# Kernel tuning notes

Measured on AMD Instinct MI355X. Metric: run time of the kernel, lower is better.

The kernel has to match this reference:

```python
import jax, jax.numpy as jnp
import numpy as np

B, N, C, H = 2, 2048, 1024, 16
HD = C // H
FF = 2 * C


def _layernorm(x, w, b, eps=1e-5):
    mu = jnp.mean(x, axis=-1, keepdims=True)
    var = jnp.var(x, axis=-1, keepdims=True)
    return (x - mu) * jax.lax.rsqrt(var + eps) * w + b


def setup_inputs() -> dict:
    key = jax.random.key(0)
    ks = jax.random.split(key, 16)
    std = 0.02
    d = {
        'q': jax.random.normal(ks[0], (B, N, C), jnp.float32),
        'k': jax.random.normal(ks[1], (B, N, C), jnp.float32),
        'v': jax.random.normal(ks[2], (B, N, C), jnp.float32),
        # attention projections (stored [in, out])
        'Wq': jax.random.normal(ks[3], (C, C), jnp.float32) * std,
        'bq': jnp.zeros((C,), jnp.float32),
        'Wk': jax.random.normal(ks[4], (C, C), jnp.float32) * std,
        'bk': jnp.zeros((C,), jnp.float32),
        'Wv': jax.random.normal(ks[5], (C, C), jnp.float32) * std,
        'bv': jnp.zeros((C,), jnp.float32),
        'Wo': jax.random.normal(ks[6], (C, C), jnp.float32) * std,
        'bo': jnp.zeros((C,), jnp.float32),
        # post-attention LayerNorm
        'ln_w': jnp.ones((C,), jnp.float32),
        'ln_b': jnp.zeros((C,), jnp.float32),
        # FFN
        'W1': jax.random.normal(ks[7], (C, FF), jnp.float32) * std,
        'b1': jnp.zeros((FF,), jnp.float32),
        'W2': jax.random.normal(ks[8], (FF, C), jnp.float32) * std,
        'b2': jnp.zeros((C,), jnp.float32),
    }
    return d


def reference(q, k, v, Wq, bq, Wk, bk, Wv, bv, Wo, bo, ln_w, ln_b, W1, b1, W2, b2):
    scale = HD ** -0.5
    # Note: the torch forward overwrites the normalized-input attention with
    # attention on raw q,k,v; only the second call affects the output.
    qh = (q @ Wq + bq).reshape(B, N, H, HD)  # [B,Nq,H,hd]
    kh = (k @ Wk + bk).reshape(B, N, H, HD)
    vh = (v @ Wv + bv).reshape(B, N, H, HD)
    attn = jnp.einsum('bqhd,bkhd->bhqk', qh, kh) * scale
    attn = jax.nn.softmax(attn, axis=-1)
    ctx = jnp.einsum('bhqk,bkhd->bqhd', attn, vh).reshape(B, N, C)
    x = ctx @ Wo + bo
    x = x + q  # residual (drop_path=0, dropout eval -> identity)
    h = _layernorm(x, ln_w, ln_b)
    y = jax.nn.gelu(h @ W1 + b1, approximate=False) @ W2 + b2
    return y + x
```

## Files before the change

kernel.cpp:

```cpp
#include <hip/hip_runtime.h>

constexpr int B_ = 2, N_ = 2048, C_ = 1024, H_ = 16, HD_ = 64, FF_ = 2048;

typedef __attribute__((ext_vector_type(8))) __bf16 bf16x8;
typedef __attribute__((ext_vector_type(4))) float f32x4;
typedef __attribute__((ext_vector_type(4))) short s16x4;

__device__ __forceinline__ unsigned short f2bf(float f) {
  union { float f; unsigned int u; } v; v.f = f;
  unsigned int r = v.u + 0x7fffu + ((v.u >> 16) & 1u);
  return (unsigned short)(r >> 16);
}

__device__ __forceinline__ void gload_lds16(const unsigned short* g, unsigned short* l) {
  __builtin_amdgcn_global_load_lds((const __attribute__((address_space(1))) void*)g,
                                   (__attribute__((address_space(3))) void*)l, 16, 0, 0);
}

__global__ __launch_bounds__(256)
void cast3_bf16(const float* __restrict__ q, const float* __restrict__ k,
                const float* __restrict__ v, unsigned short* __restrict__ qo,
                unsigned short* __restrict__ ko, unsigned short* __restrict__ vo, int n8) {
  int i = blockIdx.x * 256 + threadIdx.x;
  if (i >= n8) return;
  const float* in = blockIdx.z == 0 ? q : (blockIdx.z == 1 ? k : v);
  unsigned short* out = blockIdx.z == 0 ? qo : (blockIdx.z == 1 ? ko : vo);
  const float4 a = ((const float4*)in)[2 * i];
  const float4 b = ((const float4*)in)[2 * i + 1];
  uint4 o;
  o.x = (unsigned)f2bf(a.x) | ((unsigned)f2bf(a.y) << 16);
  o.y = (unsigned)f2bf(a.z) | ((unsigned)f2bf(a.w) << 16);
  o.z = (unsigned)f2bf(b.x) | ((unsigned)f2bf(b.y) << 16);
  o.w = (unsigned)f2bf(b.z) | ((unsigned)f2bf(b.w) << 16);
  ((uint4*)out)[i] = o;
}

__global__ __launch_bounds__(256)
void wt_cast(const float* __restrict__ W, unsigned short* __restrict__ Wt, int K, int N) {
  __shared__ unsigned short tile[32][33];
  const int tx = threadIdx.x, ty = threadIdx.y;
  const int n0 = blockIdx.x * 32, k0 = blockIdx.y * 32;
#pragma unroll
  for (int r = 0; r < 4; ++r)
    tile[ty + r * 8][tx] = f2bf(W[(size_t)(k0 + ty + r * 8) * N + n0 + tx]);
  __syncthreads();
#pragma unroll
  for (int r = 0; r < 4; ++r)
    Wt[(size_t)(n0 + ty + r * 8) * K + k0 + tx] = tile[tx][ty + r * 8];
}

__global__ __launch_bounds__(256)
void wt_cast4(const float* __restrict__ Wa, const float* __restrict__ Wb,
              const float* __restrict__ Wc, const float* __restrict__ Wd,
              unsigned short* __restrict__ Oa, unsigned short* __restrict__ Ob,
              unsigned short* __restrict__ Oc, unsigned short* __restrict__ Od) {
  __shared__ unsigned short tile[32][33];
  const int z = blockIdx.z;
  const float* W = z == 0 ? Wa : (z == 1 ? Wb : (z == 2 ? Wc : Wd));
  unsigned short* Wt = z == 0 ? Oa : (z == 1 ? Ob : (z == 2 ? Oc : Od));
  const int tx = threadIdx.x, ty = threadIdx.y;
  const int n0 = blockIdx.x * 32, k0 = blockIdx.y * 32;
#pragma unroll
  for (int r = 0; r < 4; ++r)
    tile[ty + r * 8][tx] = f2bf(W[(size_t)(k0 + ty + r * 8) * C_ + n0 + tx]);
  __syncthreads();
#pragma unroll
  for (int r = 0; r < 4; ++r)
    Wt[(size_t)(n0 + ty + r * 8) * C_ + k0 + tx] = tile[tx][ty + r * 8];
}

__global__ __launch_bounds__(256)
void vh_transpose(const unsigned short* __restrict__ Vh, unsigned short* __restrict__ VhT) {
  __shared__ unsigned short tile[32][33];
  const int tx = threadIdx.x, ty = threadIdx.y;
  const int bh = blockIdx.z, b = bh >> 4, h = bh & 15;
  const int n0 = blockIdx.x * 32, d0 = blockIdx.y * 32;
#pragma unroll
  for (int r = 0; r < 4; ++r) {
    int n = n0 + ty + r * 8;
    tile[ty + r * 8][tx] = Vh[((size_t)(b * N_ + n)) * C_ + h * HD_ + d0 + tx];
  }
  __syncthreads();
#pragma unroll
  for (int r = 0; r < 4; ++r) {
    int d = d0 + ty + r * 8;
    VhT[((size_t)(bh * HD_ + d)) * N_ + n0 + tx] = tile[tx][ty + r * 8];
  }
}

__global__ __launch_bounds__(256, 2)
void gemm_qkv(const unsigned short* __restrict__ A0, const unsigned short* __restrict__ A1,
              const unsigned short* __restrict__ A2, const unsigned short* __restrict__ B0,
              const unsigned short* __restrict__ B1, const unsigned short* __restrict__ B2,
              const float* __restrict__ c0, const float* __restrict__ c1v,
              const float* __restrict__ c2, unsigned short* __restrict__ O0,
              unsigned short* __restrict__ O1, unsigned short* __restrict__ O2) {
  const int z = blockIdx.z;
  const unsigned short* A = z == 0 ? A0 : (z == 1 ? A1 : A2);
  const unsigned short* Bt = z == 0 ? B0 : (z == 1 ? B1 : B2);
  const float* bias = z == 0 ? c0 : (z == 1 ? c1v : c2);
  unsigned short* outB = z == 0 ? O0 : (z == 1 ? O1 : O2);
  const int K = C_, Nn = C_;

  __shared__ unsigned short lA[128 * 64];
  __shared__ unsigned short lB[128 * 64];
  const int t = threadIdx.x;
  const int lane = t & 63;
  const int w = t >> 6;
  const int wm = w >> 1, wn = w & 1;
  const int l15 = lane & 15, g = lane >> 4;

  const unsigned short* Ab = A + (size_t)blockIdx.x * 128 * K;
  const unsigned short* Bb = Bt + (size_t)blockIdx.y * 128 * K;

  f32x4 acc[4][4] = {};

  for (int k0 = 0; k0 < K; k0 += 64) {
    __syncthreads();
#pragma unroll
    for (int i = 0; i < 4; ++i) {
      int id = i * 256 + t;
      gload_lds16(Ab + (size_t)(id >> 3) * K + k0 + (id & 7) * 8, &lA[id * 8]);
    }
#pragma unroll
    for (int i = 0; i < 4; ++i) {
      int id = i * 256 + t;
      gload_lds16(Bb + (size_t)(id >> 3) * K + k0 + (id & 7) * 8, &lB[id * 8]);
    }
    __syncthreads();
#pragma unroll
    for (int kk = 0; kk < 2; ++kk) {
      bf16x8 af[4], bfr[4];
#pragma unroll
      for (int mi = 0; mi < 4; ++mi)
        af[mi] = *(const bf16x8*)&lA[(wm * 64 + mi * 16 + l15) * 64 + kk * 32 + g * 8];
#pragma unroll
      for (int ni = 0; ni < 4; ++ni)
        bfr[ni] = *(const bf16x8*)&lB[(wn * 64 + ni * 16 + l15) * 64 + kk * 32 + g * 8];
#pragma unroll
      for (int mi = 0; mi < 4; ++mi)
#pragma unroll
        for (int ni = 0; ni < 4; ++ni)
          acc[mi][ni] = __builtin_amdgcn_mfma_f32_16x16x32_bf16(af[mi], bfr[ni], acc[mi][ni], 0, 0, 0);
    }
  }

#pragma unroll
  for (int mi = 0; mi < 4; ++mi)
#pragma unroll
    for (int ni = 0; ni < 4; ++ni) {
      const int col = blockIdx.y * 128 + wn * 64 + ni * 16 + l15;
      const float bcol = bias[col];
#pragma unroll
      for (int r = 0; r < 4; ++r) {
        const int row = blockIdx.x * 128 + wm * 64 + mi * 16 + g * 4 + r;
        outB[(size_t)row * Nn + col] = f2bf(acc[mi][ni][r] + bcol);
      }
    }
}

template <int EPI>
__global__ __launch_bounds__(256, 2)
void gemm_bt(const unsigned short* __restrict__ A, const unsigned short* __restrict__ Bt,
             const float* __restrict__ bias, const float* __restrict__ resid,
             float* __restrict__ outF, unsigned short* __restrict__ outB,
             int M, int N, int K) {
  __shared__ unsigned short lA[128 * 64];
  __shared__ unsigned short lB[128 * 64];
  const int t = threadIdx.x;
  const int lane = t & 63;
  const int w = t >> 6;
  const int wm = w >> 1, wn = w & 1;
  const int l15 = lane & 15, g = lane >> 4;

  const unsigned short* Ab = A + (size_t)blockIdx.x * 128 * K;
  const unsigned short* Bb = Bt + (size_t)blockIdx.y * 128 * K;

  f32x4 acc[4][4] = {};

  for (int k0 = 0; k0 < K; k0 += 64) {
    __syncthreads();
#pragma unroll
    for (int i = 0; i < 4; ++i) {
      int id = i * 256 + t;
      gload_lds16(Ab + (size_t)(id >> 3) * K + k0 + (id & 7) * 8, &lA[id * 8]);
    }
#pragma unroll
    for (int i = 0; i < 4; ++i) {
      int id = i * 256 + t;
      gload_lds16(Bb + (size_t)(id >> 3) * K + k0 + (id & 7) * 8, &lB[id * 8]);
    }
    __syncthreads();
#pragma unroll
    for (int kk = 0; kk < 2; ++kk) {
      bf16x8 af[4], bfr[4];
#pragma unroll
      for (int mi = 0; mi < 4; ++mi)
        af[mi] = *(const bf16x8*)&lA[(wm * 64 + mi * 16 + l15) * 64 + kk * 32 + g * 8];
#pragma unroll
      for (int ni = 0; ni < 4; ++ni)
        bfr[ni] = *(const bf16x8*)&lB[(wn * 64 + ni * 16 + l15) * 64 + kk * 32 + g * 8];
#pragma unroll
      for (int mi = 0; mi < 4; ++mi)
#pragma unroll
        for (int ni = 0; ni < 4; ++ni)
          acc[mi][ni] = __builtin_amdgcn_mfma_f32_16x16x32_bf16(af[mi], bfr[ni], acc[mi][ni], 0, 0, 0);
    }
  }

#pragma unroll
  for (int mi = 0; mi < 4; ++mi)
#pragma unroll
    for (int ni = 0; ni < 4; ++ni) {
      const int col = blockIdx.y * 128 + wn * 64 + ni * 16 + l15;
      const float bcol = bias[col];
#pragma unroll
      for (int r = 0; r < 4; ++r) {
        const int row = blockIdx.x * 128 + wm * 64 + mi * 16 + g * 4 + r;
        const size_t o = (size_t)row * N + col;
        float val = acc[mi][ni][r] + bcol;
        if (EPI == 0) {
          outB[o] = f2bf(val);
        } else if (EPI == 1) {
          outF[o] = val + resid[o];
        } else {
          float ge = 0.5f * val * (1.0f + erff(val * 0.70710678118654752f));
          outB[o] = f2bf(ge);
        }
      }
    }
}

__global__ __launch_bounds__(256, 2)
void gemm_n64(const unsigned short* __restrict__ A, const unsigned short* __restrict__ Bt,
              const float* __restrict__ bias, const float* __restrict__ resid,
              float* __restrict__ outF, int M, int N, int K) {
  __shared__ unsigned short lA[128 * 64];
  __shared__ unsigned short lB[64 * 64];
  const int t = threadIdx.x;
  const int lane = t & 63;
  const int w = t >> 6;
  const int wm = w >> 1, wn = w & 1;
  const int l15 = lane & 15, g = lane >> 4;

  const unsigned short* Ab = A + (size_t)blockIdx.x * 128 * K;
  const unsigned short* Bb = Bt + (size_t)blockIdx.y * 64 * K;

  f32x4 acc[4][2] = {};

  for (int k0 = 0; k0 < K; k0 += 64) {
    __syncthreads();
#pragma unroll
    for (int i = 0; i < 4; ++i) {
      int id = i * 256 + t;
      gload_lds16(Ab + (size_t)(id >> 3) * K + k0 + (id & 7) * 8, &lA[id * 8]);
    }
#pragma unroll
    for (int i = 0; i < 2; ++i) {
      int id = i * 256 + t;
      gload_lds16(Bb + (size_t)(id >> 3) * K + k0 + (id & 7) * 8, &lB[id * 8]);
    }
    __syncthreads();
#pragma unroll
    for (int kk = 0; kk < 2; ++kk) {
      bf16x8 af[4], bfr[2];
#pragma unroll
      for (int mi = 0; mi < 4; ++mi)
        af[mi] = *(const bf16x8*)&lA[(wm * 64 + mi * 16 + l15) * 64 + kk * 32 + g * 8];
#pragma unroll
      for (int ni = 0; ni < 2; ++ni)
        bfr[ni] = *(const bf16x8*)&lB[(wn * 32 + ni * 16 + l15) * 64 + kk * 32 + g * 8];
#pragma unroll
      for (int mi = 0; mi < 4; ++mi)
#pragma unroll
        for (int ni = 0; ni < 2; ++ni)
          acc[mi][ni] = __builtin_amdgcn_mfma_f32_16x16x32_bf16(af[mi], bfr[ni], acc[mi][ni], 0, 0, 0);
    }
  }

#pragma unroll
  for (int mi = 0; mi < 4; ++mi)
#pragma unroll
    for (int ni = 0; ni < 2; ++ni) {
      const int col = blockIdx.y * 64 + wn * 32 + ni * 16 + l15;
      const float bcol = bias[col];
#pragma unroll
      for (int r = 0; r < 4; ++r) {
        const int row = blockIdx.x * 128 + wm * 64 + mi * 16 + g * 4 + r;
        const size_t o = (size_t)row * N + col;
        outF[o] = acc[mi][ni][r] + bcol + resid[o];
      }
    }
}

__global__ __launch_bounds__(256, 2)
void attn_fwd(const unsigned short* __restrict__ Qh, const unsigned short* __restrict__ Kh,
              const unsigned short* __restrict__ VhT, unsigned short* __restrict__ ctx) {
  __shared__ unsigned short lK[2][64 * 64];
  __shared__ unsigned short lV[2][64 * 64];

  const int t = threadIdx.x, lane = t & 63, w = t >> 6;
  const int l15 = lane & 15, g = lane >> 4;
  const int bh = blockIdx.y, b = bh >> 4, h = bh & 15;
  const int qb0 = blockIdx.x * 128 + w * 32;

  const unsigned short* Qb = Qh + (size_t)b * N_ * C_ + h * HD_;
  const unsigned short* Kb = Kh + (size_t)b * N_ * C_ + h * HD_;
  const unsigned short* Vb = VhT + (size_t)bh * HD_ * N_;

  bf16x8 qf[2][2];
#pragma unroll
  for (int qi = 0; qi < 2; ++qi)
#pragma unroll
    for (int kk = 0; kk < 2; ++kk)
      qf[qi][kk] = *(const bf16x8*)(Qb + (size_t)(qb0 + qi * 16 + l15) * C_ + kk * 32 + g * 8);

  auto stageK = [&](int buf, int kb) {
#pragma unroll
    for (int i = 0; i < 2; ++i) {
      int o = (i * 256 + t) * 16;
      int r = o >> 7;
      int c = (o & 127) ^ ((r & 7) << 4);
      gload_lds16(Kb + (size_t)(kb + r) * C_ + (c >> 1), &lK[buf][o >> 1]);
    }
  };
  auto stageV = [&](int buf, int kb) {
#pragma unroll
    for (int i = 0; i < 2; ++i) {
      int o = (i * 256 + t) * 16;
      int r = o >> 7;
      int c = (o & 127) ^ ((r & 7) << 4);
      gload_lds16(Vb + (size_t)r * N_ + kb + (c >> 1), &lV[buf][o >> 1]);
    }
  };

  f32x4 od[4][2] = {};
  float mrun[2] = {-1e30f, -1e30f};
  float srun[2] = {0.f, 0.f};
  const float c1 = 0.18033688011112042f;
  const float DTHR = 8.0f / 0.18033688011112042f;

  stageK(0, 0);
  stageV(0, 0);
  __syncthreads();

  int cur = 0;
  for (int tile = 0; tile < N_ / 64; ++tile) {
    if (tile + 1 < N_ / 64) {
      stageK(cur ^ 1, (tile + 1) * 64);
      stageV(cur ^ 1, (tile + 1) * 64);
    }

    f32x4 st[4][2];
#pragma unroll
    for (int kf = 0; kf < 4; ++kf) {
      const int krow = kf * 16 + l15;
      const int sw = (krow & 7) << 4;
      const bf16x8 ka = *(const bf16x8*)&lK[cur][krow * 64 + ((( g * 16) ^ sw) >> 1)];
      const bf16x8 kc = *(const bf16x8*)&lK[cur][krow * 64 + (((64 + g * 16) ^ sw) >> 1)];
#pragma unroll
      for (int qi = 0; qi < 2; ++qi) {
        f32x4 z = {};
        z = __builtin_amdgcn_mfma_f32_16x16x32_bf16(ka, qf[qi][0], z, 0, 0, 0);
        z = __builtin_amdgcn_mfma_f32_16x16x32_bf16(kc, qf[qi][1], z, 0, 0, 0);
        st[kf][qi] = z;
      }
    }

    s16x4 pb[4][2];
#pragma unroll
    for (int qi = 0; qi < 2; ++qi) {
      float mx = st[0][qi][0];
#pragma unroll
      for (int r = 1; r < 4; ++r) mx = fmaxf(mx, st[0][qi][r]);
#pragma unroll
      for (int kf = 1; kf < 4; ++kf)
#pragma unroll
        for (int r = 0; r < 4; ++r) mx = fmaxf(mx, st[kf][qi][r]);
      mx = fmaxf(mx, __shfl_xor(mx, 16));
      mx = fmaxf(mx, __shfl_xor(mx, 32));
      if (__any(mx > mrun[qi] + DTHR)) {
        const float mn = fmaxf(mrun[qi], mx);
        const float sf = exp2f((mrun[qi] - mn) * c1);
        mrun[qi] = mn;
        srun[qi] *= sf;
#pragma unroll
        for (int di = 0; di < 4; ++di)
#pragma unroll
          for (int r = 0; r < 4; ++r) od[di][qi][r] *= sf;
      }
      const float mc = mrun[qi] * c1;
#pragma unroll
      for (int kf = 0; kf < 4; ++kf) {
        union { s16x4 v; __bf16 e[4]; } u;
#pragma unroll
        for (int r = 0; r < 4; ++r) {
          float pv = exp2f(st[kf][qi][r] * c1 - mc);
          srun[qi] += pv;
          u.e[r] = (__bf16)pv;
        }
        pb[kf][qi] = u.v;
      }
    }

#pragma unroll
    for (int di = 0; di < 4; ++di) {
      const int vrow = di * 16 + l15;
      const int sw = (vrow & 7) << 4;
#pragma unroll
      for (int kf = 0; kf < 4; ++kf) {
        const s16x4 vt = *(const s16x4*)&lV[cur][vrow * 64 + (((kf * 32 + g * 8) ^ sw) >> 1)];
#pragma unroll
        for (int qi = 0; qi < 2; ++qi)
          od[di][qi] = __builtin_amdgcn_mfma_f32_16x16x16bf16_1k(vt, pb[kf][qi], od[di][qi], 0, 0, 0);
      }
    }

    __syncthreads();
    cur ^= 1;
  }

#pragma unroll
  for (int qi = 0; qi < 2; ++qi) {
    float s = srun[qi];
    s += __shfl_xor(s, 16);
    s += __shfl_xor(s, 32);
    float rinv = 1.0f / s;
    const int q = qb0 + qi * 16 + l15;
#pragma unroll
    for (int di = 0; di < 4; ++di)
#pragma unroll
      for (int r = 0; r < 4; ++r) {
        int d = di * 16 + g * 4 + r;
        ctx[((size_t)(b * N_ + q)) * C_ + h * HD_ + d] = f2bf(od[di][qi][r] * rinv);
      }
  }
}

__global__ __launch_bounds__(256)
void ln_kernel(const float* __restrict__ x, const float* __restrict__ lw,
               const float* __restrict__ lb, unsigned short* __restrict__ h) {
  const int row = blockIdx.x;
  const int t = threadIdx.x;
  const float4 v = ((const float4*)(x + (size_t)row * C_))[t];
  float sum = v.x + v.y + v.z + v.w;
#pragma unroll
  for (int m = 1; m < 64; m <<= 1) sum += __shfl_xor(sum, m);
  __shared__ float red[8];
  if ((t & 63) == 0) red[t >> 6] = sum;
  __syncthreads();
  const float mu = (red[0] + red[1] + red[2] + red[3]) * (1.0f / C_);
  const float d0 = v.x - mu, d1 = v.y - mu, d2 = v.z - mu, d3 = v.w - mu;
  float sq = d0 * d0 + d1 * d1 + d2 * d2 + d3 * d3;
#pragma unroll
  for (int m = 1; m < 64; m <<= 1) sq += __shfl_xor(sq, m);
  if ((t & 63) == 0) red[4 + (t >> 6)] = sq;
  __syncthreads();
  const float var = (red[4] + red[5] + red[6] + red[7]) * (1.0f / C_);
  const float rstd = rsqrtf(var + 1e-5f);
  const float4 ww = ((const float4*)lw)[t];
  const float4 bb = ((const float4*)lb)[t];
  uint2 o;
  o.x = (unsigned)f2bf(d0 * rstd * ww.x + bb.x) | ((unsigned)f2bf(d1 * rstd * ww.y + bb.y) << 16);
  o.y = (unsigned)f2bf(d2 * rstd * ww.z + bb.z) | ((unsigned)f2bf(d3 * rstd * ww.w + bb.w) << 16);
  ((uint2*)(h + (size_t)row * C_))[t] = o;
}

extern "C" void kernel_launch(void* const* d_in, const int* in_sizes, int n_in,
                              void* d_out, int out_size, void* d_ws, size_t ws_size,
                              hipStream_t stream) {
  const float* q   = (const float*)d_in[0];
  const float* k   = (const float*)d_in[1];
  const float* v   = (const float*)d_in[2];
  const float* Wq  = (const float*)d_in[3];
  const float* bq  = (const float*)d_in[4];
  const float* Wk  = (const float*)d_in[5];
  const float* bk  = (const float*)d_in[6];
  const float* Wv  = (const float*)d_in[7];
  const float* bv  = (const float*)d_in[8];
  const float* Wo  = (const float*)d_in[9];
  const float* bo  = (const float*)d_in[10];
  const float* lnw = (const float*)d_in[11];
  const float* lnb = (const float*)d_in[12];
  const float* W1  = (const float*)d_in[13];
  const float* b1  = (const float*)d_in[14];
  const float* W2  = (const float*)d_in[15];
  const float* b2  = (const float*)d_in[16];
  float* out = (float*)d_out;

  char* ws = (char*)d_ws;
  const size_t MB = 1024 * 1024;
  if (ws_size < 120 * MB) return;
  unsigned short* qb   = (unsigned short*)(ws + 0 * MB);
  unsigned short* kb   = (unsigned short*)(ws + 8 * MB);
  unsigned short* vb   = (unsigned short*)(ws + 16 * MB);
  unsigned short* Wqt  = (unsigned short*)(ws + 24 * MB);
  unsigned short* Wkt  = (unsigned short*)(ws + 26 * MB);
  unsigned short* Wvt  = (unsigned short*)(ws + 28 * MB);
  unsigned short* Wot  = (unsigned short*)(ws + 30 * MB);
  unsigned short* W1t  = (unsigned short*)(ws + 32 * MB);
  unsigned short* W2t  = (unsigned short*)(ws + 36 * MB);
  unsigned short* Qh   = (unsigned short*)(ws + 40 * MB);
  unsigned short* Kh   = (unsigned short*)(ws + 48 * MB);
  unsigned short* Vh   = (unsigned short*)(ws + 56 * MB);
  unsigned short* VhT  = (unsigned short*)(ws + 64 * MB);
  unsigned short* ctx  = (unsigned short*)(ws + 72 * MB);
  float*          xf   = (float*)(ws + 80 * MB);
  unsigned short* hb   = (unsigned short*)(ws + 96 * MB);
  unsigned short* tbuf = (unsigned short*)(ws + 104 * MB);

  const int n8 = B_ * N_ * C_ / 8;
  cast3_bf16<<<dim3((n8 + 255) / 256, 1, 3), 256, 0, stream>>>(q, k, v, qb, kb, vb, n8);

  dim3 blk32(32, 8);
  wt_cast4<<<dim3(C_ / 32, C_ / 32, 4), blk32, 0, stream>>>(Wq, Wk, Wv, Wo, Wqt, Wkt, Wvt, Wot);
  wt_cast<<<dim3(FF_ / 32, C_ / 32), blk32, 0, stream>>>(W1, W1t, C_, FF_);
  wt_cast<<<dim3(C_ / 32, FF_ / 32), blk32, 0, stream>>>(W2, W2t, FF_, C_);

  gemm_qkv<<<dim3(B_ * N_ / 128, C_ / 128, 3), 256, 0, stream>>>(qb, kb, vb, Wqt, Wkt, Wvt,
                                                                 bq, bk, bv, Qh, Kh, Vh);

  vh_transpose<<<dim3(N_ / 32, HD_ / 32, B_ * H_), blk32, 0, stream>>>(Vh, VhT);
  attn_fwd<<<dim3(N_ / 128, B_ * H_), 256, 0, stream>>>(Qh, Kh, VhT, ctx);

  gemm_n64<<<dim3(B_ * N_ / 128, C_ / 64), 256, 0, stream>>>(ctx, Wot, bo, q, xf, B_ * N_, C_, C_);
  ln_kernel<<<dim3(B_ * N_), 256, 0, stream>>>(xf, lnw, lnb, hb);
  gemm_bt<2><<<dim3(B_ * N_ / 128, FF_ / 128), 256, 0, stream>>>(hb, W1t, b1, nullptr, nullptr, tbuf,
                                                                 B_ * N_, FF_, C_);
  gemm_n64<<<dim3(B_ * N_ / 128, C_ / 64), 256, 0, stream>>>(tbuf, W2t, b2, xf, out, B_ * N_, C_, FF_);
}
```

Measured before the change: 245.3 us.

## Double-buffer GEMM LDS tiles, add MFMA priority hints, enlarge attention blocks

All three GEMM kernels now use double-buffered LDS tiles, so the next K-slice is loaded while MFMAs run on the current one, with one barrier per iteration instead of two. s_setprio raises wave priority around the MFMA blocks in the GEMMs and in attention. The attention kernel moves to 512-thread blocks covering 256 queries, halving the K/V staging per thread and sharing each K/V tile across more waves. Its context output is written as packed 8-byte stores instead of scalar 2-byte stores. Doubling LDS per GEMM block (64KB for the 128x128 tiles) may reduce occupancy, and the larger attention blocks halve the grid size.

```diff
diff --git a/kernel.cpp b/kernel.cpp
--- a/kernel.cpp
+++ b/kernel.cpp
@@ -102,8 +102,8 @@
   unsigned short* outB = z == 0 ? O0 : (z == 1 ? O1 : O2);
   const int K = C_, Nn = C_;
 
-  __shared__ unsigned short lA[128 * 64];
-  __shared__ unsigned short lB[128 * 64];
+  __shared__ unsigned short lA[2][128 * 64];
+  __shared__ unsigned short lB[2][128 * 64];
   const int t = threadIdx.x;
   const int lane = t & 63;
   const int w = t >> 6;
@@ -113,36 +113,45 @@
   const unsigned short* Ab = A + (size_t)blockIdx.x * 128 * K;
   const unsigned short* Bb = Bt + (size_t)blockIdx.y * 128 * K;
 
-  f32x4 acc[4][4] = {};
-
-  for (int k0 = 0; k0 < K; k0 += 64) {
-    __syncthreads();
+  auto stage = [&](int buf, int k0) {
 #pragma unroll
     for (int i = 0; i < 4; ++i) {
       int id = i * 256 + t;
-      gload_lds16(Ab + (size_t)(id >> 3) * K + k0 + (id & 7) * 8, &lA[id * 8]);
+      gload_lds16(Ab + (size_t)(id >> 3) * K + k0 + (id & 7) * 8, &lA[buf][id * 8]);
     }
 #pragma unroll
     for (int i = 0; i < 4; ++i) {
       int id = i * 256 + t;
-      gload_lds16(Bb + (size_t)(id >> 3) * K + k0 + (id & 7) * 8, &lB[id * 8]);
-    }
-    __syncthreads();
+      gload_lds16(Bb + (size_t)(id >> 3) * K + k0 + (id & 7) * 8, &lB[buf][id * 8]);
+    }
+  };
+
+  f32x4 acc[4][4] = {};
+
+  stage(0, 0);
+  __syncthreads();
+  int cur = 0;
+  for (int k0 = 0; k0 < K; k0 += 64) {
+    if (k0 + 64 < K) stage(cur ^ 1, k0 + 64);
 #pragma unroll
     for (int kk = 0; kk < 2; ++kk) {
       bf16x8 af[4], bfr[4];
 #pragma unroll
       for (int mi = 0; mi < 4; ++mi)
-        af[mi] = *(const bf16x8*)&lA[(wm * 64 + mi * 16 + l15) * 64 + kk * 32 + g * 8];
+        af[mi] = *(const bf16x8*)&lA[cur][(wm * 64 + mi * 16 + l15) * 64 + kk * 32 + g * 8];
 #pragma unroll
       for (int ni = 0; ni < 4; ++ni)
-        bfr[ni] = *(const bf16x8*)&lB[(wn * 64 + ni * 16 + l15) * 64 + kk * 32 + g * 8];
+        bfr[ni] = *(const bf16x8*)&lB[cur][(wn * 64 + ni * 16 + l15) * 64 + kk * 32 + g * 8];
+      __builtin_amdgcn_s_setprio(1);
 #pragma unroll
       for (int mi = 0; mi < 4; ++mi)
 #pragma unroll
         for (int ni = 0; ni < 4; ++ni)
           acc[mi][ni] = __builtin_amdgcn_mfma_f32_16x16x32_bf16(af[mi], bfr[ni], acc[mi][ni], 0, 0, 0);
-    }
+      __builtin_amdgcn_s_setprio(0);
+    }
+    __syncthreads();
+    cur ^= 1;
   }
 
 #pragma unroll
@@ -165,8 +174,8 @@
              const float* __restrict__ bias, const float* __restrict__ resid,
              float* __restrict__ outF, unsigned short* __restrict__ outB,
              int M, int N, int K) {
-  __shared__ unsigned short lA[128 * 64];
-  __shared__ unsigned short lB[128 * 64];
+  __shared__ unsigned short lA[2][128 * 64];
+  __shared__ unsigned short lB[2][128 * 64];
   const int t = threadIdx.x;
   const int lane = t & 63;
   const int w = t >> 6;
@@ -176,36 +185,45 @@
   const unsigned short* Ab = A + (size_t)blockIdx.x * 128 * K;
   const unsigned short* Bb = Bt + (size_t)blockIdx.y * 128 * K;
 
-  f32x4 acc[4][4] = {};
-
-  for (int k0 = 0; k0 < K; k0 += 64) {
-    __syncthreads();
+  auto stage = [&](int buf, int k0) {
 #pragma unroll
     for (int i = 0; i < 4; ++i) {
       int id = i * 256 + t;
-      gload_lds16(Ab + (size_t)(id >> 3) * K + k0 + (id & 7) * 8, &lA[id * 8]);
+      gload_lds16(Ab + (size_t)(id >> 3) * K + k0 + (id & 7) * 8, &lA[buf][id * 8]);
     }
 #pragma unroll
     for (int i = 0; i < 4; ++i) {
       int id = i * 256 + t;
-      gload_lds16(Bb + (size_t)(id >> 3) * K + k0 + (id & 7) * 8, &lB[id * 8]);
-    }
-    __syncthreads();
+      gload_lds16(Bb + (size_t)(id >> 3) * K + k0 + (id & 7) * 8, &lB[buf][id * 8]);
+    }
+  };
+
+  f32x4 acc[4][4] = {};
+
+  stage(0, 0);
+  __syncthreads();
+  int cur = 0;
+  for (int k0 = 0; k0 < K; k0 += 64) {
+    if (k0 + 64 < K) stage(cur ^ 1, k0 + 64);
 #pragma unroll
     for (int kk = 0; kk < 2; ++kk) {
       bf16x8 af[4], bfr[4];
 #pragma unroll
       for (int mi = 0; mi < 4; ++mi)
-        af[mi] = *(const bf16x8*)&lA[(wm * 64 + mi * 16 + l15) * 64 + kk * 32 + g * 8];
+        af[mi] = *(const bf16x8*)&lA[cur][(wm * 64 + mi * 16 + l15) * 64 + kk * 32 + g * 8];
 #pragma unroll
       for (int ni = 0; ni < 4; ++ni)
-        bfr[ni] = *(const bf16x8*)&lB[(wn * 64 + ni * 16 + l15) * 64 + kk * 32 + g * 8];
+        bfr[ni] = *(const bf16x8*)&lB[cur][(wn * 64 + ni * 16 + l15) * 64 + kk * 32 + g * 8];
+      __builtin_amdgcn_s_setprio(1);
 #pragma unroll
       for (int mi = 0; mi < 4; ++mi)
 #pragma unroll
         for (int ni = 0; ni < 4; ++ni)
           acc[mi][ni] = __builtin_amdgcn_mfma_f32_16x16x32_bf16(af[mi], bfr[ni], acc[mi][ni], 0, 0, 0);
-    }
+      __builtin_amdgcn_s_setprio(0);
+    }
+    __syncthreads();
+    cur ^= 1;
   }
 
 #pragma unroll
@@ -235,8 +253,8 @@
 void gemm_n64(const unsigned short* __restrict__ A, const unsigned short* __restrict__ Bt,
               const float* __restrict__ bias, const float* __restrict__ resid,
               float* __restrict__ outF, int M, int N, int K) {
-  __shared__ unsigned short lA[128 * 64];
-  __shared__ unsigned short lB[64 * 64];
+  __shared__ unsigned short lA[2][128 * 64];
+  __shared__ unsigned short lB[2][64 * 64];
   const int t = threadIdx.x;
   const int lane = t & 63;
   const int w = t >> 6;
@@ -246,36 +264,45 @@
   const unsigned short* Ab = A + (size_t)blockIdx.x * 128 * K;
   const unsigned short* Bb = Bt + (size_t)blockIdx.y * 64 * K;
 
-  f32x4 acc[4][2] = {};
-
-  for (int k0 = 0; k0 < K; k0 += 64) {
-    __syncthreads();
+  auto stage = [&](int buf, int k0) {
 #pragma unroll
     for (int i = 0; i < 4; ++i) {
       int id = i * 256 + t;
-      gload_lds16(Ab + (size_t)(id >> 3) * K + k0 + (id & 7) * 8, &lA[id * 8]);
+      gload_lds16(Ab + (size_t)(id >> 3) * K + k0 + (id & 7) * 8, &lA[buf][id * 8]);
     }
 #pragma unroll
     for (int i = 0; i < 2; ++i) {
       int id = i * 256 + t;
-      gload_lds16(Bb + (size_t)(id >> 3) * K + k0 + (id & 7) * 8, &lB[id * 8]);
-    }
-    __syncthreads();
+      gload_lds16(Bb + (size_t)(id >> 3) * K + k0 + (id & 7) * 8, &lB[buf][id * 8]);
+    }
+  };
+
+  f32x4 acc[4][2] = {};
+
+  stage(0, 0);
+  __syncthreads();
+  int cur = 0;
+  for (int k0 = 0; k0 < K; k0 += 64) {
+    if (k0 + 64 < K) stage(cur ^ 1, k0 + 64);
 #pragma unroll
     for (int kk = 0; kk < 2; ++kk) {
       bf16x8 af[4], bfr[2];
 #pragma unroll
       for (int mi = 0; mi < 4; ++mi)
-        af[mi] = *(const bf16x8*)&lA[(wm * 64 + mi * 16 + l15) * 64 + kk * 32 + g * 8];
+        af[mi] = *(const bf16x8*)&lA[cur][(wm * 64 + mi * 16 + l15) * 64 + kk * 32 + g * 8];
 #pragma unroll
       for (int ni = 0; ni < 2; ++ni)
-        bfr[ni] = *(const bf16x8*)&lB[(wn * 32 + ni * 16 + l15) * 64 + kk * 32 + g * 8];
+        bfr[ni] = *(const bf16x8*)&lB[cur][(wn * 32 + ni * 16 + l15) * 64 + kk * 32 + g * 8];
+      __builtin_amdgcn_s_setprio(1);
 #pragma unroll
       for (int mi = 0; mi < 4; ++mi)
 #pragma unroll
         for (int ni = 0; ni < 2; ++ni)
           acc[mi][ni] = __builtin_amdgcn_mfma_f32_16x16x32_bf16(af[mi], bfr[ni], acc[mi][ni], 0, 0, 0);
-    }
+      __builtin_amdgcn_s_setprio(0);
+    }
+    __syncthreads();
+    cur ^= 1;
   }
 
 #pragma unroll
@@ -293,7 +320,7 @@
     }
 }
 
-__global__ __launch_bounds__(256, 2)
+__global__ __launch_bounds__(512, 2)
 void attn_fwd(const unsigned short* __restrict__ Qh, const unsigned short* __restrict__ Kh,
               const unsigned short* __restrict__ VhT, unsigned short* __restrict__ ctx) {
   __shared__ unsigned short lK[2][64 * 64];
@@ -302,7 +329,7 @@
   const int t = threadIdx.x, lane = t & 63, w = t >> 6;
   const int l15 = lane & 15, g = lane >> 4;
   const int bh = blockIdx.y, b = bh >> 4, h = bh & 15;
-  const int qb0 = blockIdx.x * 128 + w * 32;
+  const int qb0 = blockIdx.x * 256 + w * 32;
 
   const unsigned short* Qb = Qh + (size_t)b * N_ * C_ + h * HD_;
   const unsigned short* Kb = Kh + (size_t)b * N_ * C_ + h * HD_;
@@ -316,22 +343,16 @@
       qf[qi][kk] = *(const bf16x8*)(Qb + (size_t)(qb0 + qi * 16 + l15) * C_ + kk * 32 + g * 8);
 
   auto stageK = [&](int buf, int kb) {
-#pragma unroll
-    for (int i = 0; i < 2; ++i) {
-      int o = (i * 256 + t) * 16;
-      int r = o >> 7;
-      int c = (o & 127) ^ ((r & 7) << 4);
-      gload_lds16(Kb + (size_t)(kb + r) * C_ + (c >> 1), &lK[buf][o >> 1]);
-    }
+    int o = t * 16;
+    int r = o >> 7;
+    int c = (o & 127) ^ ((r & 7) << 4);
+    gload_lds16(Kb + (size_t)(kb + r) * C_ + (c >> 1), &lK[buf][o >> 1]);
   };
   auto stageV = [&](int buf, int kb) {
-#pragma unroll
-    for (int i = 0; i < 2; ++i) {
-      int o = (i * 256 + t) * 16;
-      int r = o >> 7;
-      int c = (o & 127) ^ ((r & 7) << 4);
-      gload_lds16(Vb + (size_t)r * N_ + kb + (c >> 1), &lV[buf][o >> 1]);
-    }
+    int o = t * 16;
+    int r = o >> 7;
+    int c = (o & 127) ^ ((r & 7) << 4);
+    gload_lds16(Vb + (size_t)r * N_ + kb + (c >> 1), &lV[buf][o >> 1]);
   };
 
   f32x4 od[4][2] = {};
@@ -352,6 +373,7 @@
     }
 
     f32x4 st[4][2];
+    __builtin_amdgcn_s_setprio(1);
 #pragma unroll
     for (int kf = 0; kf < 4; ++kf) {
       const int krow = kf * 16 + l15;
@@ -366,6 +388,7 @@
         st[kf][qi] = z;
       }
     }
+    __builtin_amdgcn_s_setprio(0);
 
     s16x4 pb[4][2];
 #pragma unroll
@@ -403,6 +426,7 @@
       }
     }
 
+    __builtin_amdgcn_s_setprio(1);
 #pragma unroll
     for (int di = 0; di < 4; ++di) {
       const int vrow = di * 16 + l15;
@@ -415,6 +439,7 @@
           od[di][qi] = __builtin_amdgcn_mfma_f32_16x16x16bf16_1k(vt, pb[kf][qi], od[di][qi], 0, 0, 0);
       }
     }
+    __builtin_amdgcn_s_setprio(0);
 
     __syncthreads();
     cur ^= 1;
@@ -425,15 +450,16 @@
     float s = srun[qi];
     s += __shfl_xor(s, 16);
     s += __shfl_xor(s, 32);
-    float rinv = 1.0f / s;
+    const float rinv = 1.0f / s;
     const int q = qb0 + qi * 16 + l15;
-#pragma unroll
-    for (int di = 0; di < 4; ++di)
-#pragma unroll
-      for (int r = 0; r < 4; ++r) {
-        int d = di * 16 + g * 4 + r;
-        ctx[((size_t)(b * N_ + q)) * C_ + h * HD_ + d] = f2bf(od[di][qi][r] * rinv);
-      }
+    unsigned short* cp = ctx + ((size_t)(b * N_ + q)) * C_ + h * HD_;
+#pragma unroll
+    for (int di = 0; di < 4; ++di) {
+      uint2 o;
+      o.x = (unsigned)f2bf(od[di][qi][0] * rinv) | ((unsigned)f2bf(od[di][qi][1] * rinv) << 16);
+      o.y = (unsigned)f2bf(od[di][qi][2] * rinv) | ((unsigned)f2bf(od[di][qi][3] * rinv) << 16);
+      *(uint2*)(cp + di * 16 + g * 4) = o;
+    }
   }
 }
 
@@ -521,7 +547,7 @@
                                                                  bq, bk, bv, Qh, Kh, Vh);
 
   vh_transpose<<<dim3(N_ / 32, HD_ / 32, B_ * H_), blk32, 0, stream>>>(Vh, VhT);
-  attn_fwd<<<dim3(N_ / 128, B_ * H_), 256, 0, stream>>>(Qh, Kh, VhT, ctx);
+  attn_fwd<<<dim3(N_ / 256, B_ * H_), 512, 0, stream>>>(Qh, Kh, VhT, ctx);
 
   gemm_n64<<<dim3(B_ * N_ / 128, C_ / 64), 256, 0, stream>>>(ctx, Wot, bo, q, xf, B_ * N_, C_, C_);
   ln_kernel<<<dim3(B_ * N_), 256, 0, stream>>>(xf, lnw, lnb, hb);
```

Result: slower. 251.5 us (+2.5%).
